# Kernel tuning notes

Hardware: AMD Instinct MI355X
Metric: run time of the kernel (lower is better)

The kernel has to match this reference:

```python
import jax, jax.numpy as jnp
import numpy as np

EPS = 0.1        # entropic regularization epsilon
MAX_ITER = 15    # fixed number of Sinkhorn iterations (no early stop for determinism)
TINY = 1e-16     # denominator stabilizer, matches torch code
NORM_EPS = 1e-8  # cosine-norm clamp, matches torch code


def setup_inputs() -> dict:
    key = jax.random.key(0)
    k1, k2 = jax.random.split(key)
    x = jax.random.normal(k1, (32, 512, 256), dtype=jnp.float32)
    y = jax.random.normal(k2, (32, 512, 256), dtype=jnp.float32)
    return {"x": x, "y": y}


def _cosine_distance(x, y):
    # C[b,n,m] = 1 - <x_n, y_m> / max(|x_n||y_m|, eps)
    w1 = jnp.linalg.norm(x, axis=-1, keepdims=True)            # [b,n,1]
    w2 = jnp.linalg.norm(y, axis=-1, keepdims=True)            # [b,m,1]
    dots = jnp.einsum('bnd,bmd->bnm', x, y)                    # [b,n,m]
    denom = jnp.maximum(w1 * jnp.swapaxes(w2, -2, -1), NORM_EPS)
    return 1.0 - dots / denom


def _sinkhorn(C):
    nb, n, m = C.shape
    # uniform marginals (a=None, b=None in the torch module); mask is all ones
    a = jnp.full((nb, n), 1.0 / n, dtype=C.dtype)
    b = jnp.full((nb, m), 1.0 / m, dtype=C.dtype)

    def log_K(alpha, beta):
        # log K = (-C + alpha 1^T + 1 beta^T) / eps
        return (-C + alpha[:, :, None] + beta[:, None, :]) / EPS

    def step(carry, _):
        u, v, alpha, beta = carry
        K = jnp.exp(log_K(alpha, beta))
        u = a / (jnp.einsum('bnm,bm->bn', K, v) + TINY)   # K v
        v = b / (jnp.einsum('bnm,bn->bm', K, u) + TINY)   # K^T u
        alpha = alpha + EPS * jnp.log(u)  # absorb u into log scaling
        beta = beta + EPS * jnp.log(v)    # absorb v into log scaling
        return (u, v, alpha, beta), None

    init = (jnp.ones((nb, n), C.dtype), jnp.ones((nb, m), C.dtype),
            jnp.zeros((nb, n), C.dtype), jnp.zeros((nb, m), C.dtype))
    (u, v, alpha, beta), _ = jax.lax.scan(step, init, None, length=MAX_ITER)

    # P = exp(log u + log K + log v) with the FINAL alpha/beta (as in torch code)
    pi = jnp.exp(jnp.log(u)[:, :, None] + log_K(alpha, beta) + jnp.log(v)[:, None, :])
    cost = jnp.sum(pi * C, axis=(-2, -1))  # reduction='none' -> per-batch cost [nb]
    return cost, pi, C


def reference(x, y):
    C = _cosine_distance(x, y)
    return _sinkhorn(C)
```

## Files before the change

### kernel.cpp

```cpp
#include <hip/hip_runtime.h>
#include <hip/hip_fp16.h>
#include <math.h>

#define NB 32
#define NN 512
#define DD 256
#define NROW  (NB*NN)
#define NELEM (NB*NN*DD)

constexpr float INV_EPS   = 10.0f;
constexpr float F_TINY    = 1e-16f;
constexpr float F_NORMEPS = 1e-8f;
constexpr float MARG      = 1.0f / 512.0f;

#define BARS_N 2048

typedef __attribute__((ext_vector_type(8))) short bf16x8;
typedef __attribute__((ext_vector_type(4))) float f32x4;

__device__ __forceinline__ unsigned short f2bf(float f) {
    unsigned u = __float_as_uint(f);
    u += 0x7fffu + ((u >> 16) & 1u);
    return (unsigned short)(u >> 16);
}

__global__ __launch_bounds__(256) void norms_convert(
        const float* __restrict__ x, const float* __restrict__ y,
        float* __restrict__ nx, float* __restrict__ ny,
        unsigned short* __restrict__ xh, unsigned short* __restrict__ yh,
        float* __restrict__ cost, int* __restrict__ bars) {
    if (blockIdx.x == 0) {
        if (threadIdx.x < NB) cost[threadIdx.x] = 0.0f;
        for (int i = threadIdx.x; i < BARS_N; i += 256) bars[i] = 0;
    }
    int w = threadIdx.x >> 6, l = threadIdx.x & 63;
    int row = blockIdx.x * 4 + w;
    bool isx = row < NROW;
    int r = isx ? row : row - NROW;
    const float* src = (isx ? x : y) + (size_t)r * DD;
    float4 v = ((const float4*)src)[l];
    float ss = v.x * v.x + v.y * v.y + v.z * v.z + v.w * v.w;
#pragma unroll
    for (int off = 32; off; off >>= 1) ss += __shfl_xor(ss, off);

    unsigned short* ph = (isx ? xh : yh) + (size_t)r * DD + l * 4;
    *(ushort4*)ph = make_ushort4(f2bf(v.x), f2bf(v.y), f2bf(v.z), f2bf(v.w));
    if (l == 0) (isx ? nx : ny)[r] = sqrtf(ss);
}

__global__ __launch_bounds__(256) void gemm_cos_mfma(
        const unsigned short* __restrict__ xh, const unsigned short* __restrict__ yh,
        const float* __restrict__ nx, const float* __restrict__ ny,
        float* __restrict__ C) {
    int blk = blockIdx.x;
    int b = blk >> 4, ti = (blk >> 2) & 3, tj = blk & 3;
    __shared__ short Ah[128][32], Bh[128][32];
    const unsigned short* xbh = xh + ((size_t)b * NN + ti * 128) * DD;
    const unsigned short* ybh = yh + ((size_t)b * NN + tj * 128) * DD;
    int t = threadIdx.x, w = t >> 6, l = t & 63;
    int rw = w * 32, q = l >> 4, low = l & 15;

    f32x4 acc[2][8];
#pragma unroll
    for (int i = 0; i < 2; ++i)
#pragma unroll
        for (int j = 0; j < 8; ++j) acc[i][j] = (f32x4){0.f, 0.f, 0.f, 0.f};

    int sr = t >> 1, h = t & 1;
    int c0i = 2 * h, c1i = 2 * h + 1;
    int sw0 = (c0i ^ ((sr >> 1) & 3)) * 8;
    int sw1 = (c1i ^ ((sr >> 1) & 3)) * 8;

    for (int k0 = 0; k0 < DD; k0 += 32) {
        {
            const int4* ga = (const int4*)(xbh + (size_t)sr * DD + k0);
            const int4* gc = (const int4*)(ybh + (size_t)sr * DD + k0);
            int4 a0 = ga[c0i], a1 = ga[c1i];
            int4 c0 = gc[c0i], c1 = gc[c1i];
            *(int4*)&Ah[sr][sw0] = a0; *(int4*)&Ah[sr][sw1] = a1;
            *(int4*)&Bh[sr][sw0] = c0; *(int4*)&Bh[sr][sw1] = c1;
        }
        __syncthreads();

        bf16x8 ah[2];
#pragma unroll
        for (int ti2 = 0; ti2 < 2; ++ti2) {
            int m = rw + ti2 * 16 + low;
            int pq = (q ^ ((m >> 1) & 3)) * 8;
            ah[ti2] = *(const bf16x8*)&Ah[m][pq];
        }
#pragma unroll
        for (int tj2 = 0; tj2 < 8; ++tj2) {
            int n = tj2 * 16 + low;
            int pq = (q ^ ((n >> 1) & 3)) * 8;
            bf16x8 bh = *(const bf16x8*)&Bh[n][pq];
#pragma unroll
            for (int ti2 = 0; ti2 < 2; ++ti2)
                acc[ti2][tj2] = __builtin_amdgcn_mfma_f32_16x16x32_bf16(
                    ah[ti2], bh, acc[ti2][tj2], 0, 0, 0);
        }
        __syncthreads();
    }

    float* Cb = C + (size_t)b * NN * NN;
#pragma unroll
    for (int ti2 = 0; ti2 < 2; ++ti2) {
#pragma unroll
        for (int tj2 = 0; tj2 < 8; ++tj2) {
            int gm0 = ti * 128 + rw + ti2 * 16 + q * 4;
            int gn  = tj * 128 + tj2 * 16 + low;
            float nyc = ny[b * NN + gn];
            f32x4 a = acc[ti2][tj2];
#pragma unroll
            for (int reg = 0; reg < 4; ++reg) {
                int gm = gm0 + reg;
                float d = 1.0f - a[reg] / fmaxf(nx[b * NN + gm] * nyc, F_NORMEPS);
                Cb[(size_t)gm * NN + gn] = d;
            }
        }
    }
}

__global__ __launch_bounds__(512, 2) void sink_fused(
        const float* __restrict__ C,
        float* __restrict__ cp0, float* __restrict__ cp1,
        float* __restrict__ pi, float* __restrict__ cost,
        int* __restrict__ bars) {
    int blk = blockIdx.x;
    int xcd = blk & 7, qq = blk >> 3;
    int o = qq & 7;
    int b = ((qq >> 3) << 3) | xcd;
    int tt = threadIdx.x, w = tt >> 6, l = tt & 63;
    int* flags = &bars[b * 64];

    __shared__ float sW[NN];
    __shared__ float sWP[8][NN];
    __shared__ float sPart[8];

    int4 raw[8];
    {
        const float* Cl = C + ((size_t)b * NN + o * 64 + w * 8) * NN + 8 * l;
#pragma unroll
        for (int i = 0; i < 8; ++i) {
            float4 c0 = *(const float4*)(Cl + (size_t)i * NN);
            float4 c1 = *(const float4*)(Cl + (size_t)i * NN + 4);
            __half h[8];
            h[0] = __float2half(__expf(-INV_EPS * c0.x));
            h[1] = __float2half(__expf(-INV_EPS * c0.y));
            h[2] = __float2half(__expf(-INV_EPS * c0.z));
            h[3] = __float2half(__expf(-INV_EPS * c0.w));
            h[4] = __float2half(__expf(-INV_EPS * c1.x));
            h[5] = __float2half(__expf(-INV_EPS * c1.y));
            h[6] = __float2half(__expf(-INV_EPS * c1.z));
            h[7] = __float2half(__expf(-INV_EPS * c1.w));
            raw[i] = *(const int4*)h;
        }
    }

    float A[8], Pr[8];
#pragma unroll
    for (int i = 0; i < 8; ++i) { A[i] = 1.0f; Pr[i] = 0.0f; }
    float Br = 1.0f;

    float* cpr = cp0;
    float* cpw = cp1;

    for (int t = 1; t <= 15; ++t) {
        if (t == 1) {
            sW[tt] = 1.0f;
        } else {
            if (tt < 8) {
                while (__hip_atomic_load(&flags[tt], __ATOMIC_RELAXED,
                                         __HIP_MEMORY_SCOPE_AGENT) < t - 1)
                    __builtin_amdgcn_s_sleep(1);
            }
            __syncthreads();
            float sv = 0.0f;
#pragma unroll
            for (int k = 0; k < 8; ++k)
                sv += __hip_atomic_load(
                    &cpr[(size_t)(b * 8 + k) * NN + tt],
                    __ATOMIC_RELAXED, __HIP_MEMORY_SCOPE_AGENT);
            float vv = MARG / (Br * sv + F_TINY);
            Br *= vv;
            sW[tt] = Br * vv;
        }
        __syncthreads();

        float wr[8];
        *(float4*)&wr[0] = *(const float4*)&sW[8 * l];
        *(float4*)&wr[4] = *(const float4*)&sW[8 * l + 4];

        float p[8];
#pragma unroll
        for (int e = 0; e < 8; ++e) p[e] = 0.0f;
#pragma unroll
        for (int i = 0; i < 8; ++i) {
            const __half* hv = (const __half*)&raw[i];
            float f0 = __half2float(hv[0]), f1 = __half2float(hv[1]);
            float f2 = __half2float(hv[2]), f3 = __half2float(hv[3]);
            float f4 = __half2float(hv[4]), f5 = __half2float(hv[5]);
            float f6 = __half2float(hv[6]), f7 = __half2float(hv[7]);
            float s = 0.0f;
            s = fmaf(f0, wr[0], s); s = fmaf(f1, wr[1], s);
            s = fmaf(f2, wr[2], s); s = fmaf(f3, wr[3], s);
            s = fmaf(f4, wr[4], s); s = fmaf(f5, wr[5], s);
            s = fmaf(f6, wr[6], s); s = fmaf(f7, wr[7], s);
#pragma unroll
            for (int off = 32; off; off >>= 1) s += __shfl_xor(s, off);
            float uu = MARG / (A[i] * s + F_TINY);
            A[i] *= uu;
            if (t == 15) Pr[i] = A[i] * uu;
            float ai = A[i];
            p[0] = fmaf(f0, ai, p[0]); p[1] = fmaf(f1, ai, p[1]);
            p[2] = fmaf(f2, ai, p[2]); p[3] = fmaf(f3, ai, p[3]);
            p[4] = fmaf(f4, ai, p[4]); p[5] = fmaf(f5, ai, p[5]);
            p[6] = fmaf(f6, ai, p[6]); p[7] = fmaf(f7, ai, p[7]);
        }
        *(float4*)&sWP[w][8 * l]     = make_float4(p[0], p[1], p[2], p[3]);
        *(float4*)&sWP[w][8 * l + 4] = make_float4(p[4], p[5], p[6], p[7]);
        __syncthreads();
        float cs = 0.0f;
#pragma unroll
        for (int ww = 0; ww < 8; ++ww) cs += sWP[ww][tt];
        cpw[(size_t)(b * 8 + o) * NN + tt] = cs;

        __syncthreads();
        if (tt == 0)
            __hip_atomic_store(&flags[o], t, __ATOMIC_RELAXED,
                               __HIP_MEMORY_SCOPE_AGENT);

        float* tmp = cpr; cpr = cpw; cpw = tmp;
    }

    if (tt < 8) {
        while (__hip_atomic_load(&flags[tt], __ATOMIC_RELAXED,
                                 __HIP_MEMORY_SCOPE_AGENT) < 15)
            __builtin_amdgcn_s_sleep(1);
    }
    __syncthreads();
    {
        float sv = 0.0f;
#pragma unroll
        for (int k = 0; k < 8; ++k)
            sv += __hip_atomic_load(
                &cpr[(size_t)(b * 8 + k) * NN + tt],
                __ATOMIC_RELAXED, __HIP_MEMORY_SCOPE_AGENT);
        float vv = MARG / (Br * sv + F_TINY);
        sW[tt] = Br * vv * vv;
    }
    __syncthreads();

    float q0[8];
    *(float4*)&q0[0] = *(const float4*)&sW[4 * l];
    *(float4*)&q0[4] = *(const float4*)&sW[256 + 4 * l];
    const float* Cb = C + (size_t)b * NN * NN;
    float* pib = pi + (size_t)b * NN * NN;
    float csum = 0.0f;
#pragma unroll 2
    for (int i = 0; i < 8; ++i) {
        int r = o * 64 + w * 8 + i;
        float pf = Pr[i];
        const float* crow = Cb + (size_t)r * NN;
        float* prow = pib + (size_t)r * NN;
        float4 c0 = *(const float4*)(crow + 4 * l);
        float4 c1 = *(const float4*)(crow + 256 + 4 * l);
        float pv0 = pf * q0[0] * __expf(-INV_EPS * c0.x);
        float pv1 = pf * q0[1] * __expf(-INV_EPS * c0.y);
        float pv2 = pf * q0[2] * __expf(-INV_EPS * c0.z);
        float pv3 = pf * q0[3] * __expf(-INV_EPS * c0.w);
        float pv4 = pf * q0[4] * __expf(-INV_EPS * c1.x);
        float pv5 = pf * q0[5] * __expf(-INV_EPS * c1.y);
        float pv6 = pf * q0[6] * __expf(-INV_EPS * c1.z);
        float pv7 = pf * q0[7] * __expf(-INV_EPS * c1.w);
        *(float4*)(prow + 4 * l)       = make_float4(pv0, pv1, pv2, pv3);
        *(float4*)(prow + 256 + 4 * l) = make_float4(pv4, pv5, pv6, pv7);
        csum = fmaf(pv0, c0.x, csum); csum = fmaf(pv1, c0.y, csum);
        csum = fmaf(pv2, c0.z, csum); csum = fmaf(pv3, c0.w, csum);
        csum = fmaf(pv4, c1.x, csum); csum = fmaf(pv5, c1.y, csum);
        csum = fmaf(pv6, c1.z, csum); csum = fmaf(pv7, c1.w, csum);
    }
#pragma unroll
    for (int off = 32; off; off >>= 1) csum += __shfl_xor(csum, off);
    if (l == 0) sPart[w] = csum;
    __syncthreads();
    if (tt == 0) {
        float tot = 0.0f;
#pragma unroll
        for (int ww = 0; ww < 8; ++ww) tot += sPart[ww];
        atomicAdd(&cost[b], tot);
    }
}

extern "C" void kernel_launch(void* const* d_in, const int* in_sizes, int n_in,
                              void* d_out, int out_size, void* d_ws, size_t ws_size,
                              hipStream_t stream) {
    const float* x = (const float*)d_in[0];
    const float* y = (const float*)d_in[1];
    float* out  = (float*)d_out;
    float* cost = out;
    float* pi   = out + 32;
    float* C    = out + 32 + (size_t)NB * NN * NN;

    float* ws = (float*)d_ws;
    float* nx = ws;
    float* ny = ws + 16384;
    int*  bars = (int*)(ws + 32768);
    unsigned short* xh = (unsigned short*)(ws + 65536);
    unsigned short* yh = xh + NELEM;
    float* cp0 = (float*)(yh + NELEM);
    float* cp1 = cp0 + (size_t)NB * 8 * NN;

    norms_convert<<<dim3(8192), dim3(256), 0, stream>>>(
        x, y, nx, ny, xh, yh, cost, bars);
    gemm_cos_mfma<<<dim3(512), dim3(256), 0, stream>>>(
        xh, yh, nx, ny, C);

    const float* C_p = C;
    float* cp0_p = cp0; float* cp1_p = cp1;
    float* pi_p = pi; float* cost_p = cost; int* bars_p = bars;
    void* args[] = { &C_p, &cp0_p, &cp1_p, &pi_p, &cost_p, &bars_p };
    hipLaunchCooperativeKernel(reinterpret_cast<void*>(sink_fused),
                               dim3(256), dim3(512), args, 0, stream);
}
```

Baseline: 184.4 us.

## Fuse norm computation and bf16 conversion into cosine GEMM kernel

Removes the separate norms_convert kernel and instead has the GEMM load fp32 x/y tiles directly, convert them to bf16 in registers, and accumulate squared norms along the K loop. Norms are reduced per row into shared memory and used in the epilogue. This removes one launch and the write and reread of the bf16 copies and norms. In exchange, each GEMM block reads fp32 data (twice the bytes), and every x/y row is re-read and re-converted by four tiles.

```diff
diff --git a/kernel.cpp b/kernel.cpp
--- a/kernel.cpp
+++ b/kernel.cpp
@@ -5,8 +5,6 @@
 #define NB 32
 #define NN 512
 #define DD 256
-#define NROW  (NB*NN)
-#define NELEM (NB*NN*DD)
 
 constexpr float INV_EPS   = 10.0f;
 constexpr float F_TINY    = 1e-16f;
@@ -23,40 +21,24 @@
     u += 0x7fffu + ((u >> 16) & 1u);
     return (unsigned short)(u >> 16);
 }
-
-__global__ __launch_bounds__(256) void norms_convert(
+__device__ __forceinline__ int pack2(float a, float b) {
+    return (int)f2bf(a) | ((int)f2bf(b) << 16);
+}
+
+__global__ __launch_bounds__(256) void gemm_cos_mfma(
         const float* __restrict__ x, const float* __restrict__ y,
-        float* __restrict__ nx, float* __restrict__ ny,
-        unsigned short* __restrict__ xh, unsigned short* __restrict__ yh,
-        float* __restrict__ cost, int* __restrict__ bars) {
-    if (blockIdx.x == 0) {
+        float* __restrict__ C, float* __restrict__ cost,
+        int* __restrict__ bars) {
+    int blk = blockIdx.x;
+    int b = blk >> 4, ti = (blk >> 2) & 3, tj = blk & 3;
+    if (blk == 0) {
         if (threadIdx.x < NB) cost[threadIdx.x] = 0.0f;
         for (int i = threadIdx.x; i < BARS_N; i += 256) bars[i] = 0;
     }
-    int w = threadIdx.x >> 6, l = threadIdx.x & 63;
-    int row = blockIdx.x * 4 + w;
-    bool isx = row < NROW;
-    int r = isx ? row : row - NROW;
-    const float* src = (isx ? x : y) + (size_t)r * DD;
-    float4 v = ((const float4*)src)[l];
-    float ss = v.x * v.x + v.y * v.y + v.z * v.z + v.w * v.w;
-#pragma unroll
-    for (int off = 32; off; off >>= 1) ss += __shfl_xor(ss, off);
-
-    unsigned short* ph = (isx ? xh : yh) + (size_t)r * DD + l * 4;
-    *(ushort4*)ph = make_ushort4(f2bf(v.x), f2bf(v.y), f2bf(v.z), f2bf(v.w));
-    if (l == 0) (isx ? nx : ny)[r] = sqrtf(ss);
-}
-
-__global__ __launch_bounds__(256) void gemm_cos_mfma(
-        const unsigned short* __restrict__ xh, const unsigned short* __restrict__ yh,
-        const float* __restrict__ nx, const float* __restrict__ ny,
-        float* __restrict__ C) {
-    int blk = blockIdx.x;
-    int b = blk >> 4, ti = (blk >> 2) & 3, tj = blk & 3;
     __shared__ short Ah[128][32], Bh[128][32];
-    const unsigned short* xbh = xh + ((size_t)b * NN + ti * 128) * DD;
-    const unsigned short* ybh = yh + ((size_t)b * NN + tj * 128) * DD;
+    __shared__ float sNx[128], sNy[128];
+    const float* xb = x + ((size_t)b * NN + ti * 128) * DD;
+    const float* yb = y + ((size_t)b * NN + tj * 128) * DD;
     int t = threadIdx.x, w = t >> 6, l = t & 63;
     int rw = w * 32, q = l >> 4, low = l & 15;
 
@@ -70,15 +52,32 @@
     int c0i = 2 * h, c1i = 2 * h + 1;
     int sw0 = (c0i ^ ((sr >> 1) & 3)) * 8;
     int sw1 = (c1i ^ ((sr >> 1) & 3)) * 8;
+    float ssA = 0.0f, ssB = 0.0f;
 
     for (int k0 = 0; k0 < DD; k0 += 32) {
         {
-            const int4* ga = (const int4*)(xbh + (size_t)sr * DD + k0);
-            const int4* gc = (const int4*)(ybh + (size_t)sr * DD + k0);
-            int4 a0 = ga[c0i], a1 = ga[c1i];
-            int4 c0 = gc[c0i], c1 = gc[c1i];
-            *(int4*)&Ah[sr][sw0] = a0; *(int4*)&Ah[sr][sw1] = a1;
-            *(int4*)&Bh[sr][sw0] = c0; *(int4*)&Bh[sr][sw1] = c1;
+            const float4* ga = (const float4*)(xb + (size_t)sr * DD + k0 + 16 * h);
+            const float4* gc = (const float4*)(yb + (size_t)sr * DD + k0 + 16 * h);
+            float4 a0 = ga[0], a1 = ga[1], a2 = ga[2], a3 = ga[3];
+            float4 c0 = gc[0], c1 = gc[1], c2 = gc[2], c3 = gc[3];
+            ssA += a0.x*a0.x + a0.y*a0.y + a0.z*a0.z + a0.w*a0.w;
+            ssA += a1.x*a1.x + a1.y*a1.y + a1.z*a1.z + a1.w*a1.w;
+            ssA += a2.x*a2.x + a2.y*a2.y + a2.z*a2.z + a2.w*a2.w;
+            ssA += a3.x*a3.x + a3.y*a3.y + a3.z*a3.z + a3.w*a3.w;
+            ssB += c0.x*c0.x + c0.y*c0.y + c0.z*c0.z + c0.w*c0.w;
+            ssB += c1.x*c1.x + c1.y*c1.y + c1.z*c1.z + c1.w*c1.w;
+            ssB += c2.x*c2.x + c2.y*c2.y + c2.z*c2.z + c2.w*c2.w;
+            ssB += c3.x*c3.x + c3.y*c3.y + c3.z*c3.z + c3.w*c3.w;
+            int4 pa0 = { pack2(a0.x,a0.y), pack2(a0.z,a0.w),
+                         pack2(a1.x,a1.y), pack2(a1.z,a1.w) };
+            int4 pa1 = { pack2(a2.x,a2.y), pack2(a2.z,a2.w),
+                         pack2(a3.x,a3.y), pack2(a3.z,a3.w) };
+            int4 pc0 = { pack2(c0.x,c0.y), pack2(c0.z,c0.w),
+                         pack2(c1.x,c1.y), pack2(c1.z,c1.w) };
+            int4 pc1 = { pack2(c2.x,c2.y), pack2(c2.z,c2.w),
+                         pack2(c3.x,c3.y), pack2(c3.z,c3.w) };
+            *(int4*)&Ah[sr][sw0] = pa0; *(int4*)&Ah[sr][sw1] = pa1;
+            *(int4*)&Bh[sr][sw0] = pc0; *(int4*)&Bh[sr][sw1] = pc1;
         }
         __syncthreads();
 
@@ -102,19 +101,26 @@
         __syncthreads();
     }
 
+    float tA = ssA + __shfl_xor(ssA, 1);
+    float tB = ssB + __shfl_xor(ssB, 1);
+    if (h == 0) { sNx[sr] = sqrtf(tA); sNy[sr] = sqrtf(tB); }
+    __syncthreads();
+
     float* Cb = C + (size_t)b * NN * NN;
 #pragma unroll
     for (int ti2 = 0; ti2 < 2; ++ti2) {
 #pragma unroll
         for (int tj2 = 0; tj2 < 8; ++tj2) {
-            int gm0 = ti * 128 + rw + ti2 * 16 + q * 4;
-            int gn  = tj * 128 + tj2 * 16 + low;
-            float nyc = ny[b * NN + gn];
+            int ml0 = rw + ti2 * 16 + q * 4;
+            int nl  = tj2 * 16 + low;
+            int gm0 = ti * 128 + ml0;
+            int gn  = tj * 128 + nl;
+            float nyc = sNy[nl];
             f32x4 a = acc[ti2][tj2];
 #pragma unroll
             for (int reg = 0; reg < 4; ++reg) {
                 int gm = gm0 + reg;
-                float d = 1.0f - a[reg] / fmaxf(nx[b * NN + gm] * nyc, F_NORMEPS);
+                float d = 1.0f - a[reg] / fmaxf(sNx[ml0 + reg] * nyc, F_NORMEPS);
                 Cb[(size_t)gm * NN + gn] = d;
             }
         }
@@ -302,19 +308,12 @@
     float* pi   = out + 32;
     float* C    = out + 32 + (size_t)NB * NN * NN;
 
-    float* ws = (float*)d_ws;
-    float* nx = ws;
-    float* ny = ws + 16384;
-    int*  bars = (int*)(ws + 32768);
-    unsigned short* xh = (unsigned short*)(ws + 65536);
-    unsigned short* yh = xh + NELEM;
-    float* cp0 = (float*)(yh + NELEM);
+    int* bars = (int*)d_ws;
+    float* cp0 = (float*)((char*)d_ws + 8192);
     float* cp1 = cp0 + (size_t)NB * 8 * NN;
 
-    norms_convert<<<dim3(8192), dim3(256), 0, stream>>>(
-        x, y, nx, ny, xh, yh, cost, bars);
     gemm_cos_mfma<<<dim3(512), dim3(256), 0, stream>>>(
-        xh, yh, nx, ny, C);
+        x, y, C, cost, bars);
 
     const float* C_p = C;
     float* cp0_p = cp0; float* cp1_p = cp1;
```

Result: faster. 174.9 us, median of 2 (-5.2%).
